# Performance work log

Measured on AMD Instinct MI355X. Metric: run time of the kernel, lower is better.

The kernel has to match this reference:

```python
import jax, jax.numpy as jnp
import numpy as np
import math

B, S = 4, 1024
V, D, L, H, F, MAXLEN = 32000, 1024, 6, 16, 4096, 2048
DH = D // H
NUM_BUCKETS, MAX_DIST = 32, 256
REL_SCALE = 64.0 ** 0.5
EPS = 1e-5


def setup_inputs() -> dict:
    key = jax.random.key(0)
    ks = iter(jax.random.split(key, 32))
    sd = 0.02
    inp = {
        'src': jax.random.randint(next(ks), (B, S), 0, V),
        'src_mask': jnp.ones((B, 1, 1, S), dtype=jnp.int32),
        'tok_emb': jax.random.normal(next(ks), (V, D), jnp.float32) * sd,
        'pos_emb': jax.random.normal(next(ks), (MAXLEN, D), jnp.float32) * sd,
        'Wq': jax.random.normal(next(ks), (L, D, D), jnp.float32) * sd,
        'bq': jnp.zeros((L, D), jnp.float32),
        'Wk': jax.random.normal(next(ks), (L, D, D), jnp.float32) * sd,
        'bk': jnp.zeros((L, D), jnp.float32),
        'Wv': jax.random.normal(next(ks), (L, D, D), jnp.float32) * sd,
        'bv': jnp.zeros((L, D), jnp.float32),
        'Wo': jax.random.normal(next(ks), (L, D, D), jnp.float32) * sd,
        'bo': jnp.zeros((L, D), jnp.float32),
        'rel_bias': jax.random.normal(next(ks), (L, NUM_BUCKETS, H), jnp.float32) * sd,
        'ln1_g': jnp.ones((L, D), jnp.float32),
        'ln1_b': jnp.zeros((L, D), jnp.float32),
        'W1': jax.random.normal(next(ks), (L, D, F), jnp.float32) * sd,
        'b1': jnp.zeros((L, F), jnp.float32),
        'W2': jax.random.normal(next(ks), (L, F, D), jnp.float32) * sd,
        'b2': jnp.zeros((L, D), jnp.float32),
        'ln2_g': jnp.ones((L, D), jnp.float32),
        'ln2_b': jnp.zeros((L, D), jnp.float32),
    }
    return inp


def _rel_pos_bucket(seq_len):
    # non-causal bucketing (T5-style), matching the torch source
    q = jnp.arange(seq_len)
    k = jnp.arange(seq_len)
    n = q[:, None] - k[None, :]          # == -(k - q)
    nb = NUM_BUCKETS // 2                # 16
    ret = (n < 0).astype(jnp.int32) * nb
    n = jnp.abs(n)
    max_exact = nb // 2                  # 8
    is_small = n < max_exact
    val_large = max_exact + (
        jnp.log(jnp.maximum(n, 1).astype(jnp.float32) / max_exact)
        / math.log(MAX_DIST / max_exact) * (nb - max_exact)
    ).astype(jnp.int32)
    val_large = jnp.minimum(val_large, nb - 1)
    return ret + jnp.where(is_small, n, val_large)  # [S,S] in [0,32)


def _layer_norm(x, g, b):
    mu = jnp.mean(x, axis=-1, keepdims=True)
    var = jnp.var(x, axis=-1, keepdims=True)
    return (x - mu) * jax.lax.rsqrt(var + EPS) * g + b


def reference(src, src_mask, tok_emb, pos_emb, Wq, bq, Wk, bk, Wv, bv, Wo, bo,
              rel_bias, ln1_g, ln1_b, W1, b1, W2, b2, ln2_g, ln2_b):
    seq_len = src.shape[1]
    bucket = _rel_pos_bucket(seq_len)                      # [S,S] int
    x = tok_emb[src] * jnp.sqrt(jnp.float32(D)) + pos_emb[jnp.arange(seq_len)][None]
    scale = jnp.sqrt(jnp.float32(DH))
    neg = jnp.float32(-1e10)

    def layer(x, p):
        (wq, bq_, wk, bk_, wv, bv_, wo, bo_, rb, g1, b1_, w1, bb1, w2, bb2, g2, b2_) = p
        Q = (x @ wq + bq_).reshape(B, seq_len, H, DH)
        K = (x @ wk + bk_).reshape(B, seq_len, H, DH)
        Vv = (x @ wv + bv_).reshape(B, seq_len, H, DH)
        energy = jnp.einsum('bqhd,bkhd->bhqk', Q, K) / scale
        energy = jnp.where(src_mask == 0, neg, energy)
        bias = rb[bucket]                                  # [S,S,H]
        energy = energy + jnp.transpose(bias, (2, 0, 1))[None] * REL_SCALE
        attn = jax.nn.softmax(energy, axis=-1)
        o = jnp.einsum('bhqk,bkhd->bqhd', attn, Vv).reshape(B, seq_len, D)
        o = o @ wo + bo_
        x = _layer_norm(x + o, g1, b1_)
        f = jax.nn.relu(x @ w1 + bb1) @ w2 + bb2
        x = _layer_norm(x + f, g2, b2_)
        return x, None

    params = (Wq, bq, Wk, bk, Wv, bv, Wo, bo, rel_bias,
              ln1_g, ln1_b, W1, b1, W2, b2, ln2_g, ln2_b)
    x, _ = jax.lax.scan(layer, x, params)
    return x
```

## Files before the change

### kernel.cpp

```cpp
#include <hip/hip_runtime.h>

#define B_ 4
#define S_ 1024
#define D_ 1024
#define F_ 4096
#define H_ 16
#define L_ 6
#define M_ (B_*S_)

#define LOG2E 1.44269504088896f

typedef unsigned short u16;
typedef __attribute__((ext_vector_type(4))) unsigned short u16x4;
typedef __attribute__((ext_vector_type(8))) short s16x8;
typedef __attribute__((ext_vector_type(8))) __bf16 bf16x8;
typedef __attribute__((ext_vector_type(4))) float f32x4;

typedef const __attribute__((address_space(1))) unsigned int gu32;
typedef __attribute__((address_space(3))) unsigned int su32;

__device__ __forceinline__ u16 f2bf(float f) {
  union { float f; unsigned u; } v; v.f = f;
  unsigned u = v.u;
  return (u16)((u + 0x7fffu + ((u >> 16) & 1u)) >> 16);
}
__device__ __forceinline__ float bf2f(u16 h) {
  union { unsigned u; float f; } v; v.u = (unsigned)h << 16; return v.f;
}

__device__ __forceinline__ f32x4 mfma16(s16x8 a, s16x8 b, f32x4 c) {
  return __builtin_amdgcn_mfma_f32_16x16x32_bf16(
      __builtin_bit_cast(bf16x8, a), __builtin_bit_cast(bf16x8, b), c, 0, 0, 0);
}

__device__ __forceinline__ void gload16(const void* g, void* s) {
  __builtin_amdgcn_global_load_lds((gu32*)g, (su32*)s, 16, 0, 0);
}

template<int OUTMODE>
__device__ __forceinline__ void gemm128_body(
    const u16* __restrict__ A, const u16* __restrict__ Bt,
    const float* __restrict__ b0, const float* __restrict__ b1,
    const float* __restrict__ b2, u16* __restrict__ Ch,
    u16* __restrict__ Vt, int N, int K, int kbeg, int kend)
{
  __shared__ __align__(16) u16 As[128 * 64];
  __shared__ __align__(16) u16 Bs[128 * 64];
  const int tid = threadIdx.x, lane = tid & 63, w = tid >> 6;
  const int bm = blockIdx.x * 128, bn = blockIdx.y * 128;
  const int wm = (w >> 1) * 64, wn = (w & 1) * 64;

  f32x4 acc[4][4];
#pragma unroll
  for (int i = 0; i < 4; i++)
#pragma unroll
    for (int j = 0; j < 4; j++) acc[i][j] = {0.f, 0.f, 0.f, 0.f};

  for (int k0 = kbeg; k0 < kend; k0 += 64) {
    __syncthreads();
#pragma unroll
    for (int i = 0; i < 4; i++) {
      const int flat = i * 4096 + w * 1024 + lane * 16;
      const int row = flat >> 7, ce = (flat & 127) >> 1;
      gload16(A + (size_t)(bm + row) * K + k0 + ce, As + i * 2048 + w * 512);
      gload16(Bt + (size_t)(bn + row) * K + k0 + ce, Bs + i * 2048 + w * 512);
    }
    __syncthreads();
#pragma unroll
    for (int kk = 0; kk < 2; kk++) {
      s16x8 af[4], bf[4];
#pragma unroll
      for (int mf = 0; mf < 4; mf++)
        af[mf] = *(const s16x8*)&As[(wm + mf * 16 + (lane & 15)) * 64 + kk * 32 + (lane >> 4) * 8];
#pragma unroll
      for (int nf = 0; nf < 4; nf++)
        bf[nf] = *(const s16x8*)&Bs[(wn + nf * 16 + (lane & 15)) * 64 + kk * 32 + (lane >> 4) * 8];
#pragma unroll
      for (int mf = 0; mf < 4; mf++)
#pragma unroll
        for (int nf = 0; nf < 4; nf++)
          acc[mf][nf] = mfma16(af[mf], bf[nf], acc[mf][nf]);
    }
  }

  if (OUTMODE == 3) {
    const int zz = bn >> 10;
    const int lcb = (bn & 1023) + wn;
    const float* bp = (zz == 0) ? b0 : (zz == 1) ? b1 : b2;
    if (zz == 2) {
      const int b = bm >> 10;
#pragma unroll
      for (int nf = 0; nf < 4; nf++) {
        const int dh2 = lcb + nf * 16 + (lane & 15);
        const int hq = dh2 >> 6, dh = dh2 & 63;
        const float bv = bp[dh2];
        u16* vrow = Vt + ((size_t)((b << 4) + hq) * 64 + dh) * S_;
#pragma unroll
        for (int mf = 0; mf < 4; mf++) {
          const int s0 = (bm & 1023) + wm + mf * 16 + ((lane >> 4) << 2);
          u16x4 hv;
#pragma unroll
          for (int j = 0; j < 4; j++) hv[j] = f2bf(acc[mf][nf][j] + bv);
          *(u16x4*)(vrow + s0) = hv;
        }
      }
    } else {
      const float sc = (zz == 0) ? (0.125f * LOG2E) : 1.0f;
      u16* Outz = Ch + (size_t)zz * M_ * D_;
#pragma unroll
      for (int nf = 0; nf < 4; nf++) {
        const int col = lcb + nf * 16 + (lane & 15);
        const float bv = bp[col];
#pragma unroll
        for (int mf = 0; mf < 4; mf++) {
#pragma unroll
          for (int j = 0; j < 4; j++) {
            const int row = bm + wm + mf * 16 + ((lane >> 4) << 2) + j;
            Outz[(size_t)row * D_ + col] = f2bf((acc[mf][nf][j] + bv) * sc);
          }
        }
      }
    }
  } else {
#pragma unroll
    for (int nf = 0; nf < 4; nf++) {
      const int col = bn + wn + nf * 16 + (lane & 15);
#pragma unroll
      for (int mf = 0; mf < 4; mf++) {
#pragma unroll
        for (int j = 0; j < 4; j++) {
          const int row = bm + wm + mf * 16 + ((lane >> 4) << 2) + j;
          Ch[(size_t)row * N + col] = f2bf(acc[mf][nf][j]);
        }
      }
    }
  }
}

__global__ __launch_bounds__(256, 3) void gemm_qkvf(
    const u16* __restrict__ A, const u16* __restrict__ WT,
    const float* __restrict__ bq, const float* __restrict__ bk,
    const float* __restrict__ bv, u16* __restrict__ Out, u16* __restrict__ Vt)
{
  gemm128_body<3>(A, WT, bq, bk, bv, Out, Vt, 3 * D_, D_, 0, D_);
}

__global__ __launch_bounds__(256, 3) void gemm_osplit2(
    const u16* __restrict__ A, const u16* __restrict__ WT,
    u16* __restrict__ P)
{
  const int z = blockIdx.z;
  gemm128_body<1>(A, WT, nullptr, nullptr, nullptr,
                  P + (size_t)z * M_ * D_, nullptr, D_, D_, z * 512, z * 512 + 512);
}

__device__ __forceinline__ s16x8 readfrag(const u16* half, int r, int kk, int hi4) {
  const int c = (kk * 64 + hi4 * 16) ^ ((r & 7) << 4);
  return *(const s16x8*)((const char*)half + r * 128 + c);
}

__device__ __forceinline__ void stage_half(
    const u16* __restrict__ src, int ldk, u16* lds_half, int w, int lane)
{
#pragma unroll
  for (int j = 0; j < 2; j++) {
    const int flat = j * 8192 + w * 1024 + lane * 16;
    const int row = flat >> 7;
    const int kb = (flat & 127) ^ ((row & 7) << 4);
    gload16(src + (size_t)row * ldk + (kb >> 1), lds_half + j * 4096 + w * 512);
  }
}

#define BAR     asm volatile("s_barrier" ::: "memory")
#define PH_PRE  asm volatile("s_barrier" ::: "memory"); __builtin_amdgcn_s_setprio(1)
#define PH_POST __builtin_amdgcn_s_setprio(0); __builtin_amdgcn_sched_barrier(0)
#define VM4     asm volatile("s_waitcnt vmcnt(4)" ::: "memory")
#define VM0     asm volatile("s_waitcnt vmcnt(0)" ::: "memory")

#define READ_B(bufhalf) do { \
  _Pragma("unroll") for (int nf = 0; nf < 4; nf++) \
  _Pragma("unroll") for (int kk = 0; kk < 2; kk++) \
    bfr[nf][kk] = readfrag(bufhalf, rb0 + nf * 16 + lo16, kk, hi4); } while (0)
#define READ_A(bufhalf, Q) do { \
  _Pragma("unroll") for (int m = 0; m < 2; m++) \
  _Pragma("unroll") for (int kk = 0; kk < 2; kk++) \
    af[m][kk] = readfrag(bufhalf, (2 * (Q) + m) * 16 + lo16, kk, hi4); } while (0)
#define DO_MFMA(Q) do { \
  _Pragma("unroll") for (int kk = 0; kk < 2; kk++) \
  _Pragma("unroll") for (int m = 0; m < 2; m++) \
  _Pragma("unroll") for (int nf = 0; nf < 4; nf++) \
    acc[2 * (Q) + m][nf] = mfma16(af[m][kk], bfr[nf][kk], acc[2 * (Q) + m][nf]); } while (0)

template<int OUTMODE>
__device__ __forceinline__ void gemm256_body(
    const u16* __restrict__ A, const u16* __restrict__ Bt,
    const float* __restrict__ bias, u16* __restrict__ Ch,
    int N, int K, int kbeg, int kslice)
{
  __shared__ __align__(16) u16 As[2][2][8192];
  __shared__ __align__(16) u16 Bs[2][2][8192];
  const int tid = threadIdx.x, lane = tid & 63, w = tid >> 6;
  const int wr = w >> 2, wc = w & 3;
  const int lo16 = lane & 15, hi4 = lane >> 4;
  const int bm = blockIdx.x * 256, bn = blockIdx.y * 256;
  const int rb0 = (wc & 1) * 64;

  const u16* Abase = A + (size_t)bm * K + kbeg;
  const u16* Bbase = Bt + (size_t)bn * K + kbeg;
  const size_t h1 = (size_t)128 * K;
  const int NT = kslice >> 6, NI = NT >> 1;

  f32x4 acc[8][4];
#pragma unroll
  for (int i = 0; i < 8; i++)
#pragma unroll
    for (int j = 0; j < 4; j++) acc[i][j] = {0.f, 0.f, 0.f, 0.f};

  stage_half(Abase,           K, As[0][0], w, lane);
  stage_half(Abase + h1,      K, As[0][1], w, lane);
  stage_half(Bbase,           K, Bs[0][0], w, lane);
  stage_half(Bbase + h1,      K, Bs[0][1], w, lane);
  stage_half(Abase + 64,      K, As[1][0], w, lane);
  stage_half(Abase + h1 + 64, K, As[1][1], w, lane);
  stage_half(Bbase + 64,      K, Bs[1][0], w, lane);
  stage_half(Bbase + h1 + 64, K, Bs[1][1], w, lane);
  asm volatile("s_waitcnt vmcnt(8)" ::: "memory");
  BAR;

  const u16* Ae = As[0][wr]; const u16* Ao = As[1][wr];
  const u16* Be = Bs[0][wc >> 1]; const u16* Bo = Bs[1][wc >> 1];
  s16x8 af[2][2], bfr[4][2];

  for (int it = 0; it < NI - 1; ++it) {
    READ_B(Be); READ_A(Ae, 0);
    if (it > 0) {
      stage_half(Abase +      (size_t)(2 * it + 1) * 64, K, As[1][0], w, lane);
      stage_half(Abase + h1 + (size_t)(2 * it + 1) * 64, K, As[1][1], w, lane);
    }
    PH_PRE; DO_MFMA(0); PH_POST; BAR;
    READ_A(Ae, 1);
    stage_half(Bbase +      (size_t)(2 * it + 2) * 64, K, Bs[0][0], w, lane);
    PH_PRE; DO_MFMA(1); PH_POST; BAR;
    READ_A(Ae, 2);
    stage_half(Bbase + h1 + (size_t)(2 * it + 2) * 64, K, Bs[0][1], w, lane);
    PH_PRE; DO_MFMA(2); PH_POST; BAR;
    READ_A(Ae, 3);
    PH_PRE; DO_MFMA(3); PH_POST; VM4; BAR;
    READ_B(Bo); READ_A(Ao, 0);
    stage_half(Abase +      (size_t)(2 * it + 2) * 64, K, As[0][0], w, lane);
    stage_half(Abase + h1 + (size_t)(2 * it + 2) * 64, K, As[0][1], w, lane);
    PH_PRE; DO_MFMA(0); PH_POST; BAR;
    READ_A(Ao, 1);
    stage_half(Bbase +      (size_t)(2 * it + 3) * 64, K, Bs[1][0], w, lane);
    PH_PRE; DO_MFMA(1); PH_POST; BAR;
    READ_A(Ao, 2);
    stage_half(Bbase + h1 + (size_t)(2 * it + 3) * 64, K, Bs[1][1], w, lane);
    PH_PRE; DO_MFMA(2); PH_POST; BAR;
    READ_A(Ao, 3);
    PH_PRE; DO_MFMA(3); PH_POST; VM4; BAR;
  }
  READ_B(Be); READ_A(Ae, 0);
  stage_half(Abase +      (size_t)(NT - 1) * 64, K, As[1][0], w, lane);
  stage_half(Abase + h1 + (size_t)(NT - 1) * 64, K, As[1][1], w, lane);
  PH_PRE; DO_MFMA(0); PH_POST; BAR;
  READ_A(Ae, 1);             PH_PRE; DO_MFMA(1); PH_POST; BAR;
  READ_A(Ae, 2);             PH_PRE; DO_MFMA(2); PH_POST; BAR;
  READ_A(Ae, 3);             PH_PRE; DO_MFMA(3); PH_POST; VM0; BAR;
  READ_B(Bo); READ_A(Ao, 0); PH_PRE; DO_MFMA(0); PH_POST; BAR;
  READ_A(Ao, 1);             PH_PRE; DO_MFMA(1); PH_POST; BAR;
  READ_A(Ao, 2);             PH_PRE; DO_MFMA(2); PH_POST; BAR;
  READ_A(Ao, 3);             PH_PRE; DO_MFMA(3); PH_POST;

  const int row0 = bm + wr * 128, col0 = bn + wc * 64;
#pragma unroll
  for (int nf = 0; nf < 4; nf++) {
    const int col = col0 + nf * 16 + lo16;
    const float bv = (OUTMODE == 2) ? bias[col] : 0.f;
#pragma unroll
    for (int mf = 0; mf < 8; mf++) {
#pragma unroll
      for (int j = 0; j < 4; j++) {
        const int row = row0 + mf * 16 + hi4 * 4 + j;
        float v = acc[mf][nf][j];
        if (OUTMODE == 2) v = fmaxf(v + bv, 0.f);
        Ch[(size_t)row * N + col] = f2bf(v);
      }
    }
  }
}

__global__ __launch_bounds__(512, 2) void gemm_ffn1(
    const u16* __restrict__ A, const u16* __restrict__ WT,
    const float* __restrict__ bias, u16* __restrict__ Out)
{
  gemm256_body<2>(A, WT, bias, Out, F_, D_, 0, D_);
}

__global__ __launch_bounds__(512, 2) void gemm_ffn2sp4(
    const u16* __restrict__ A, const u16* __restrict__ WT,
    u16* __restrict__ P)
{
  const int z = blockIdx.z;
  gemm256_body<4>(A, WT, nullptr, P + (size_t)z * M_ * D_,
                  D_, F_, z * 1024, 1024);
}

__global__ __launch_bounds__(256) void transpose_layer(
    const float* __restrict__ Wq, const float* __restrict__ Wk,
    const float* __restrict__ Wv, const float* __restrict__ Wo,
    const float* __restrict__ W1, const float* __restrict__ W2,
    u16* __restrict__ WT)
{
  __shared__ float tl[64][65];
  int bt = blockIdx.x;
  const float* src; u16* dst; int Rsrc, Csrc, cx, cy;
  if (bt < 1024) {
    const int m = bt >> 8; const int t = bt & 255;
    src = (m == 0) ? Wq : (m == 1) ? Wk : (m == 2) ? Wv : Wo;
    dst = WT + (size_t)m * 1024 * 1024;
    Rsrc = 1024; Csrc = 1024; cx = t & 15; cy = t >> 4;
  } else if (bt < 2048) {
    const int t = bt - 1024;
    src = W1; dst = WT + (size_t)4 * 1024 * 1024;
    Rsrc = 1024; Csrc = 4096; cx = t & 63; cy = t >> 6;
  } else {
    const int t = bt - 2048;
    src = W2; dst = WT + (size_t)8 * 1024 * 1024;
    Rsrc = 4096; Csrc = 1024; cx = t & 15; cy = t >> 4;
  }
  const int r0 = cy * 64, c0 = cx * 64;
  const int tid = threadIdx.x;
  const int rl = tid >> 2, q = tid & 3;
  const float* sp = src + (size_t)(r0 + rl) * Csrc + c0 + q * 16;
#pragma unroll
  for (int i = 0; i < 4; i++) {
    const float4 v = *(const float4*)(sp + i * 4);
    tl[rl][q * 16 + i * 4 + 0] = v.x;
    tl[rl][q * 16 + i * 4 + 1] = v.y;
    tl[rl][q * 16 + i * 4 + 2] = v.z;
    tl[rl][q * 16 + i * 4 + 3] = v.w;
  }
  __syncthreads();
#pragma unroll
  for (int it = 0; it < 2; it++) {
    const int idx = tid + it * 256;
    const int cl = idx >> 3, seg = idx & 7;
    const int rw0 = seg * 8;
    s16x8 v8;
#pragma unroll
    for (int u = 0; u < 8; u++) v8[u] = (short)f2bf(tl[rw0 + u][cl]);
    *(s16x8*)(dst + (size_t)(c0 + cl) * Rsrc + r0 + rw0) = v8;
  }
}

__global__ __launch_bounds__(256) void build_lut(
    const float* __restrict__ rb, float* __restrict__ lut_g)
{
  const int h = blockIdx.x, l = blockIdx.y;
  for (int idx = threadIdx.x; idx < 2048; idx += 256) {
    const int rel = idx - 1024;
    const int ret = rel < 0 ? 16 : 0;
    const int n = rel < 0 ? -rel : rel;
    int bu;
    if (n < 8) bu = ret + n;
    else {
      const float t = logf((float)n * 0.125f) * (8.0f / 3.4657359027997265f);
      int vl = 8 + (int)t;
      if (vl > 15) vl = 15;
      bu = ret + vl;
    }
    lut_g[(size_t)(l * H_ + h) * 2048 + idx] = rb[l * 512 + bu * 16 + h] * (8.0f * LOG2E);
  }
}

__global__ __launch_bounds__(256) void mask2neg(
    const int* __restrict__ mask, u16* __restrict__ mf)
{
  const int i = blockIdx.x * 256 + threadIdx.x;
  if (i < B_ * S_) mf[i] = mask[i] ? (u16)0 : f2bf(-1e10f * LOG2E);
}

__device__ __forceinline__ s16x8 lds_swz(const u16* base, int row, int cb) {
  const int addr = row * 128 + (cb ^ ((row & 7) << 4));
  return *(const s16x8*)((const char*)base + addr);
}

#define ATTN_STAGE(t, buf) do { \
  const int kt2 = (t) * 64; \
  const int flat2 = tid * 16; \
  const int row2 = flat2 >> 7; \
  const int ce2 = ((flat2 & 127) ^ ((row2 & 7) << 4)) >> 1; \
  gload16(Kb + (size_t)(bS + kt2 + row2) * D_ + hh + ce2, Ks[buf] + w * 512); \
  gload16(Vt + (size_t)(bh * 64 + row2) * S_ + kt2 + ce2, Vs[buf] + w * 512); \
} while (0)

#define ATTN_TILE(bc, kt) do { \
    f32x4 sacc[4]; \
    _Pragma("unroll") for (int i = 0; i < 4; i++) sacc[i] = {0.f, 0.f, 0.f, 0.f}; \
    __builtin_amdgcn_s_setprio(1); \
    _Pragma("unroll") for (int kk = 0; kk < 2; kk++) { \
      const int cb = kk * 64 + hi4 * 16; \
      _Pragma("unroll") for (int nf = 0; nf < 4; nf++) { \
        const s16x8 kb = lds_swz(Ks[bc], nf * 16 + lo16, cb); \
        sacc[nf] = mfma16(qf[kk], kb, sacc[nf]); \
      } \
    } \
    __builtin_amdgcn_s_setprio(0); \
    float kmf[4]; \
    _Pragma("unroll") for (int nf = 0; nf < 4; nf++) \
      kmf[nf] = bf2f(maskf[(kt) + nf * 16 + lo16]); \
    const int lidx0 = q0 + hi4 * 4 + 1024 - (kt) - lo16; \
    _Pragma("unroll") for (int j = 0; j < 4; j++) { \
      const int lrow = (hi4 << 2) + j; \
      _Pragma("unroll") for (int nf = 0; nf < 4; nf++) { \
        const float s = sacc[nf][j] + kmf[nf] + lut[lidx0 + j - nf * 16]; \
        Ps[w][lrow * 68 + nf * 16 + lo16] = f2bf(__builtin_amdgcn_exp2f(s)); \
      } \
    } \
    __builtin_amdgcn_s_setprio(1); \
    _Pragma("unroll") for (int kk = 0; kk < 2; kk++) { \
      const s16x8 pa = *(const s16x8*)&Ps[w][lo16 * 68 + kk * 32 + hi4 * 8]; \
      const int cb = kk * 64 + hi4 * 16; \
      _Pragma("unroll") for (int df = 0; df < 4; df++) { \
        const s16x8 vb = lds_swz(Vs[bc], df * 16 + lo16, cb); \
        oacc[df] = mfma16(pa, vb, oacc[df]); \
      } \
      oacc[4] = mfma16(pa, onesf, oacc[4]); \
    } \
    __builtin_amdgcn_s_setprio(0); \
} while (0)

__global__ __launch_bounds__(512, 2) void attn_kernel(
    const u16* __restrict__ Qb, const u16* __restrict__ Kb,
    const u16* __restrict__ Vt, const u16* __restrict__ mask16,
    const float* __restrict__ lut_g, u16* __restrict__ AO)
{
  __shared__ __align__(16) float lut[2048];
  __shared__ __align__(16) u16 maskf[1024];
  __shared__ __align__(16) u16 Ks[3][64 * 64];
  __shared__ __align__(16) u16 Vs[3][64 * 64];
  __shared__ __align__(16) u16 Ps[8][16 * 68];

  const int tid = threadIdx.x;
  const int lane = tid & 63;
  const int w = tid >> 6;
  const int bh = blockIdx.x;
  const int b = bh >> 4, h = bh & 15;
  const int q0 = blockIdx.y * 128 + w * 16;
  const int bS = b * S_, hh = h * 64;
  const int lo16 = lane & 15, hi4 = lane >> 4;

  const float* lsrc = lut_g + (size_t)h * 2048;
  gload16(lsrc + w * 256 + lane * 4, lut + w * 256);
  if (w < 2)
    gload16(mask16 + bS + w * 512 + lane * 8, maskf + w * 512);

  s16x8 qf[2];
#pragma unroll
  for (int kk = 0; kk < 2; kk++)
    qf[kk] = *(const s16x8*)(Qb + (size_t)(bS + q0 + lo16) * D_ + hh +
                             kk * 32 + hi4 * 8);

  s16x8 onesf;
#pragma unroll
  for (int u = 0; u < 8; u++) onesf[u] = (short)((lo16 == 0) ? 0x3F80 : 0);

  f32x4 oacc[5];
#pragma unroll
  for (int i = 0; i < 5; i++) oacc[i] = {0.f, 0.f, 0.f, 0.f};

  ATTN_STAGE(0, 0);
  ATTN_STAGE(1, 1);

  for (int t = 0; t < S_ / 64 - 1; ++t) {
    const int bc = t % 3;
    const int kt = t * 64;
    asm volatile("s_waitcnt vmcnt(2)" ::: "memory");
    __builtin_amdgcn_s_barrier();
    if (t + 2 < S_ / 64) ATTN_STAGE(t + 2, (t + 2) % 3);
    ATTN_TILE(bc, kt);
  }
  {
    const int t = S_ / 64 - 1;
    asm volatile("s_waitcnt vmcnt(0)" ::: "memory");
    __builtin_amdgcn_s_barrier();
    ATTN_TILE(t % 3, t * 64);
  }

  float inv[4];
#pragma unroll
  for (int j = 0; j < 4; j++) {
    const float l = __shfl(oacc[4][j], lane & 48);
    inv[j] = 1.0f / l;
  }
#pragma unroll
  for (int df = 0; df < 4; df++)
#pragma unroll
    for (int j = 0; j < 4; j++) {
      const int qrow = q0 + (hi4 << 2) + j;
      AO[(size_t)(bS + qrow) * D_ + hh + df * 16 + lo16] =
          f2bf(oacc[df][j] * inv[j]);
    }
}

template<int NP>
__global__ __launch_bounds__(256) void ln_fusedb(
    const u16* __restrict__ Xh, const u16* __restrict__ P,
    const float* __restrict__ bias, const float* __restrict__ g,
    const float* __restrict__ be, u16* __restrict__ Yh, float* __restrict__ Yf)
{
  const int row = blockIdx.x;
  const int tid = threadIdx.x;
  const size_t off = (size_t)row * D_;
  const size_t ps = (size_t)M_ * D_;
  const u16x4 xv = ((const u16x4*)(Xh + off))[tid];
  float v[4];
#pragma unroll
  for (int q = 0; q < 4; q++) v[q] = bf2f(xv[q]);
#pragma unroll
  for (int p = 0; p < NP; p++) {
    const u16x4 pv = ((const u16x4*)(P + p * ps + off))[tid];
#pragma unroll
    for (int q = 0; q < 4; q++) v[q] += bf2f(pv[q]);
  }
  const float4 bb = ((const float4*)bias)[tid];
  v[0] += bb.x; v[1] += bb.y; v[2] += bb.z; v[3] += bb.w;

  float sum = v[0] + v[1] + v[2] + v[3];
  float ss = v[0] * v[0] + v[1] * v[1] + v[2] * v[2] + v[3] * v[3];
#pragma unroll
  for (int o = 1; o < 64; o <<= 1) {
    sum += __shfl_xor(sum, o);
    ss += __shfl_xor(ss, o);
  }
  __shared__ float s1[4], s2[4];
  if ((tid & 63) == 0) { s1[tid >> 6] = sum; s2[tid >> 6] = ss; }
  __syncthreads();
  sum = s1[0] + s1[1] + s1[2] + s1[3];
  ss = s2[0] + s2[1] + s2[2] + s2[3];
  const float mu = sum * (1.f / D_);
  const float var = ss * (1.f / D_) - mu * mu;
  const float rstd = rsqrtf(var + 1e-5f);
  const float4 gv = ((const float4*)g)[tid];
  const float4 bv = ((const float4*)be)[tid];
  float y[4];
  y[0] = (v[0] - mu) * rstd * gv.x + bv.x;
  y[1] = (v[1] - mu) * rstd * gv.y + bv.y;
  y[2] = (v[2] - mu) * rstd * gv.z + bv.z;
  y[3] = (v[3] - mu) * rstd * gv.w + bv.w;
  u16x4 hv;
  hv.x = f2bf(y[0]); hv.y = f2bf(y[1]); hv.z = f2bf(y[2]); hv.w = f2bf(y[3]);
  ((u16x4*)(Yh + off))[tid] = hv;
  if (Yf != nullptr) {
    float4 yf; yf.x = y[0]; yf.y = y[1]; yf.z = y[2]; yf.w = y[3];
    ((float4*)(Yf + off))[tid] = yf;
  }
}

__global__ __launch_bounds__(256) void embed_kernel(
    const int* __restrict__ src, const float* __restrict__ tok,
    const float* __restrict__ pos, u16* __restrict__ Xh)
{
  const int row = blockIdx.x;
  const int s = row & (S_ - 1);
  const int t = src[row];
  const int tid = threadIdx.x;
  const float4 tv = ((const float4*)(tok + (size_t)t * D_))[tid];
  const float4 pv = ((const float4*)(pos + (size_t)s * D_))[tid];
  u16x4 hv;
  hv.x = f2bf(tv.x * 32.f + pv.x);
  hv.y = f2bf(tv.y * 32.f + pv.y);
  hv.z = f2bf(tv.z * 32.f + pv.z);
  hv.w = f2bf(tv.w * 32.f + pv.w);
  ((u16x4*)(Xh + (size_t)row * D_))[tid] = hv;
}

extern "C" void kernel_launch(void* const* d_in, const int* in_sizes, int n_in,
                              void* d_out, int out_size, void* d_ws, size_t ws_size,
                              hipStream_t stream)
{
  const int* src = (const int*)d_in[0];
  const int* mask = (const int*)d_in[1];
  const float* tok_emb = (const float*)d_in[2];
  const float* pos_emb = (const float*)d_in[3];
  const float* Wq = (const float*)d_in[4];
  const float* bq = (const float*)d_in[5];
  const float* Wk = (const float*)d_in[6];
  const float* bk = (const float*)d_in[7];
  const float* Wv = (const float*)d_in[8];
  const float* bv = (const float*)d_in[9];
  const float* Wo = (const float*)d_in[10];
  const float* bo = (const float*)d_in[11];
  const float* rb = (const float*)d_in[12];
  const float* g1 = (const float*)d_in[13];
  const float* b1n = (const float*)d_in[14];
  const float* W1 = (const float*)d_in[15];
  const float* b1f = (const float*)d_in[16];
  const float* W2 = (const float*)d_in[17];
  const float* b2f = (const float*)d_in[18];
  const float* g2 = (const float*)d_in[19];
  const float* b2n = (const float*)d_in[20];
  float* out = (float*)d_out;

  char* ws = (char*)d_ws;
  const size_t MB = 1ull << 20;
  u16* xb16  = (u16*)(ws + 0);
  u16* Qb16  = (u16*)(ws + 8 * MB);
  u16* Kb16  = (u16*)(ws + 16 * MB);
  u16* Vt16  = (u16*)(ws + 24 * MB);
  u16* AO16  = (u16*)(ws + 32 * MB);
  u16* Pp16  = (u16*)(ws + 40 * MB);
  u16* WT    = (u16*)(ws + 72 * MB);
  u16* Hb16  = (u16*)(ws + 8 * MB);
  float* lut_g  = (float*)(ws + 96 * MB);
  u16*   mask16 = (u16*)(ws + 96 * MB + 786432);

  u16* WTqkv = WT;
  u16* WTo   = WT + (size_t)3 * 1024 * 1024;
  u16* WT1   = WT + (size_t)4 * 1024 * 1024;
  u16* WT2   = WT + (size_t)8 * 1024 * 1024;

  embed_kernel<<<M_, 256, 0, stream>>>(src, tok_emb, pos_emb, xb16);
  build_lut<<<dim3(H_, L_), 256, 0, stream>>>(rb, lut_g);
  mask2neg<<<(B_ * S_ + 255) / 256, 256, 0, stream>>>(mask, mask16);

  for (int l = 0; l < L_; l++) {
    const size_t oDD = (size_t)l * D_ * D_;
    const size_t oDF = (size_t)l * D_ * F_;

    transpose_layer<<<3072, 256, 0, stream>>>(
        Wq + oDD, Wk + oDD, Wv + oDD, Wo + oDD, W1 + oDF, W2 + oDF, WT);

    gemm_qkvf<<<dim3(M_ / 128, 3 * D_ / 128), 256, 0, stream>>>(
        xb16, WTqkv, bq + l * D_, bk + l * D_, bv + l * D_, Qb16, Vt16);

    attn_kernel<<<dim3(B_ * H_, S_ / 128), 512, 0, stream>>>(
        Qb16, Kb16, Vt16, mask16, lut_g + (size_t)l * H_ * 2048, AO16);

    gemm_osplit2<<<dim3(M_ / 128, D_ / 128, 2), 256, 0, stream>>>(
        AO16, WTo, Pp16);

    ln_fusedb<2><<<M_, 256, 0, stream>>>(
        xb16, Pp16, bo + l * D_, g1 + l * D_, b1n + l * D_, xb16, nullptr);

    gemm_ffn1<<<dim3(M_ / 256, F_ / 256), 512, 0, stream>>>(
        xb16, WT1, b1f + l * F_, Hb16);

    gemm_ffn2sp4<<<dim3(M_ / 256, D_ / 256, 4), 512, 0, stream>>>(
        Hb16, WT2, Pp16);

    ln_fusedb<4><<<M_, 256, 0, stream>>>(
        xb16, Pp16, b2f + l * D_, g2 + l * D_, b2n + l * D_, xb16,
        (l == L_ - 1) ? out : nullptr);
  }
}
```

Measured before the change: 1.233 ms.

## Replace 128x128 QKV/out-proj GEMM with pipelined 256x128 double-buffered tile

The QKV and output-projection GEMMs move from a simple 128x128 tile, which synchronises twice per K step with no prefetch, to a 256x128 tile run by 512 threads. The new body double-buffers LDS with swizzled staging and overlaps the next tile's global-to-LDS loads with MFMA phases, using barriers and setprio. This is meant to hide load latency and raise reuse of operands per byte loaded. In exchange it needs more LDS per block and allows fewer resident blocks, and the grid has half as many blocks, which may hurt wave balance across CUs.

Measured after the change: 1.261 ms. 2.3% more time.

```diff
diff --git a/kernel.cpp b/kernel.cpp
--- a/kernel.cpp
+++ b/kernel.cpp
@@ -37,18 +37,65 @@
   __builtin_amdgcn_global_load_lds((gu32*)g, (su32*)s, 16, 0, 0);
 }
 
+__device__ __forceinline__ s16x8 readfrag(const u16* half, int r, int kk, int hi4) {
+  const int c = (kk * 64 + hi4 * 16) ^ ((r & 7) << 4);
+  return *(const s16x8*)((const char*)half + r * 128 + c);
+}
+
+__device__ __forceinline__ void stage_half(
+    const u16* __restrict__ src, int ldk, u16* lds_half, int w, int lane)
+{
+#pragma unroll
+  for (int j = 0; j < 2; j++) {
+    const int flat = j * 8192 + w * 1024 + lane * 16;
+    const int row = flat >> 7;
+    const int kb = (flat & 127) ^ ((row & 7) << 4);
+    gload16(src + (size_t)row * ldk + (kb >> 1), lds_half + j * 4096 + w * 512);
+  }
+}
+
+#define BAR     asm volatile("s_barrier" ::: "memory")
+#define PH_PRE  asm volatile("s_barrier" ::: "memory"); __builtin_amdgcn_s_setprio(1)
+#define PH_POST __builtin_amdgcn_s_setprio(0); __builtin_amdgcn_sched_barrier(0)
+#define VM0     asm volatile("s_waitcnt vmcnt(0)" ::: "memory")
+#define VM2     asm volatile("s_waitcnt vmcnt(2)" ::: "memory")
+#define VM4     asm volatile("s_waitcnt vmcnt(4)" ::: "memory")
+
+#define READ_BX(buf) do { \
+  _Pragma("unroll") for (int nf = 0; nf < 4; nf++) \
+  _Pragma("unroll") for (int kk = 0; kk < 2; kk++) \
+    bfr[nf][kk] = readfrag(buf, rb0 + nf * 16 + lo16, kk, hi4); } while (0)
+#define READ_AX(buf, Q0) do { \
+  _Pragma("unroll") for (int m = 0; m < 2; m++) \
+  _Pragma("unroll") for (int kk = 0; kk < 2; kk++) \
+    af[m][kk] = readfrag(buf, ar0 + ((Q0) + m) * 16 + lo16, kk, hi4); } while (0)
+#define DO_MFMAX(Q0) do { \
+  _Pragma("unroll") for (int kk = 0; kk < 2; kk++) \
+  _Pragma("unroll") for (int m = 0; m < 2; m++) \
+  _Pragma("unroll") for (int nf = 0; nf < 4; nf++) \
+    acc[(Q0) + m][nf] = mfma16(af[m][kk], bfr[nf][kk], acc[(Q0) + m][nf]); } while (0)
+
 template<int OUTMODE>
-__device__ __forceinline__ void gemm128_body(
+__device__ __forceinline__ void gemm256x128_body(
     const u16* __restrict__ A, const u16* __restrict__ Bt,
     const float* __restrict__ b0, const float* __restrict__ b1,
     const float* __restrict__ b2, u16* __restrict__ Ch,
-    u16* __restrict__ Vt, int N, int K, int kbeg, int kend)
-{
-  __shared__ __align__(16) u16 As[128 * 64];
-  __shared__ __align__(16) u16 Bs[128 * 64];
+    u16* __restrict__ Vt, int N, int K, int kbeg, int kslice)
+{
+  __shared__ __align__(16) u16 As[2][2][8192];
+  __shared__ __align__(16) u16 Bs[2][8192];
   const int tid = threadIdx.x, lane = tid & 63, w = tid >> 6;
-  const int bm = blockIdx.x * 128, bn = blockIdx.y * 128;
-  const int wm = (w >> 1) * 64, wn = (w & 1) * 64;
+  const int wr = w >> 1, wc = w & 1;
+  const int lo16 = lane & 15, hi4 = lane >> 4;
+  const int bm = blockIdx.x * 256, bn = blockIdx.y * 128;
+  const int ah = wr >> 1;
+  const int ar0 = (wr & 1) * 64;
+  const int rb0 = wc * 64;
+
+  const u16* Abase = A + (size_t)bm * K + kbeg;
+  const u16* Bbase = Bt + (size_t)bn * K + kbeg;
+  const size_t h1 = (size_t)128 * K;
+  const int NT = kslice >> 6, NI = NT >> 1;
 
   f32x4 acc[4][4];
 #pragma unroll
@@ -56,48 +103,62 @@
 #pragma unroll
     for (int j = 0; j < 4; j++) acc[i][j] = {0.f, 0.f, 0.f, 0.f};
 
-  for (int k0 = kbeg; k0 < kend; k0 += 64) {
-    __syncthreads();
-#pragma unroll
-    for (int i = 0; i < 4; i++) {
-      const int flat = i * 4096 + w * 1024 + lane * 16;
-      const int row = flat >> 7, ce = (flat & 127) >> 1;
-      gload16(A + (size_t)(bm + row) * K + k0 + ce, As + i * 2048 + w * 512);
-      gload16(Bt + (size_t)(bn + row) * K + k0 + ce, Bs + i * 2048 + w * 512);
+  stage_half(Abase,           K, As[0][0], w, lane);
+  stage_half(Abase + h1,      K, As[0][1], w, lane);
+  stage_half(Bbase,           K, Bs[0],    w, lane);
+  stage_half(Abase + 64,      K, As[1][0], w, lane);
+  stage_half(Abase + h1 + 64, K, As[1][1], w, lane);
+  stage_half(Bbase + 64,      K, Bs[1],    w, lane);
+  asm volatile("s_waitcnt vmcnt(6)" ::: "memory");
+  BAR;
+
+  s16x8 af[2][2], bfr[4][2];
+
+  for (int it = 0; it < NI - 1; ++it) {
+    READ_BX(Bs[0]); READ_AX(As[0][ah], 0);
+    if (it > 0) {
+      stage_half(Abase +      (size_t)(2 * it + 1) * 64, K, As[1][0], w, lane);
+      stage_half(Abase + h1 + (size_t)(2 * it + 1) * 64, K, As[1][1], w, lane);
     }
-    __syncthreads();
-#pragma unroll
-    for (int kk = 0; kk < 2; kk++) {
-      s16x8 af[4], bf[4];
-#pragma unroll
-      for (int mf = 0; mf < 4; mf++)
-        af[mf] = *(const s16x8*)&As[(wm + mf * 16 + (lane & 15)) * 64 + kk * 32 + (lane >> 4) * 8];
-#pragma unroll
-      for (int nf = 0; nf < 4; nf++)
-        bf[nf] = *(const s16x8*)&Bs[(wn + nf * 16 + (lane & 15)) * 64 + kk * 32 + (lane >> 4) * 8];
-#pragma unroll
-      for (int mf = 0; mf < 4; mf++)
-#pragma unroll
-        for (int nf = 0; nf < 4; nf++)
-          acc[mf][nf] = mfma16(af[mf], bf[nf], acc[mf][nf]);
-    }
-  }
-
+    PH_PRE; DO_MFMAX(0); PH_POST; BAR;
+    READ_AX(As[0][ah], 2);
+    stage_half(Bbase + (size_t)(2 * it + 2) * 64, K, Bs[0], w, lane);
+    PH_PRE; DO_MFMAX(2); PH_POST; VM2; BAR;
+    READ_BX(Bs[1]); READ_AX(As[1][ah], 0);
+    stage_half(Abase +      (size_t)(2 * it + 2) * 64, K, As[0][0], w, lane);
+    stage_half(Abase + h1 + (size_t)(2 * it + 2) * 64, K, As[0][1], w, lane);
+    PH_PRE; DO_MFMAX(0); PH_POST; BAR;
+    READ_AX(As[1][ah], 2);
+    stage_half(Bbase + (size_t)(2 * it + 3) * 64, K, Bs[1], w, lane);
+    PH_PRE; DO_MFMAX(2); PH_POST; VM2; BAR;
+  }
+  READ_BX(Bs[0]); READ_AX(As[0][ah], 0);
+  stage_half(Abase +      (size_t)(NT - 1) * 64, K, As[1][0], w, lane);
+  stage_half(Abase + h1 + (size_t)(NT - 1) * 64, K, As[1][1], w, lane);
+  PH_PRE; DO_MFMAX(0); PH_POST; BAR;
+  READ_AX(As[0][ah], 2);
+  PH_PRE; DO_MFMAX(2); PH_POST; VM0; BAR;
+  READ_BX(Bs[1]); READ_AX(As[1][ah], 0);
+  PH_PRE; DO_MFMAX(0); PH_POST; BAR;
+  READ_AX(As[1][ah], 2);
+  PH_PRE; DO_MFMAX(2); PH_POST;
+
+  const int row0 = bm + wr * 64;
   if (OUTMODE == 3) {
     const int zz = bn >> 10;
-    const int lcb = (bn & 1023) + wn;
+    const int lcb = (bn & 1023) + wc * 64;
     const float* bp = (zz == 0) ? b0 : (zz == 1) ? b1 : b2;
     if (zz == 2) {
       const int b = bm >> 10;
 #pragma unroll
       for (int nf = 0; nf < 4; nf++) {
-        const int dh2 = lcb + nf * 16 + (lane & 15);
+        const int dh2 = lcb + nf * 16 + lo16;
         const int hq = dh2 >> 6, dh = dh2 & 63;
         const float bv = bp[dh2];
         u16* vrow = Vt + ((size_t)((b << 4) + hq) * 64 + dh) * S_;
 #pragma unroll
         for (int mf = 0; mf < 4; mf++) {
-          const int s0 = (bm & 1023) + wm + mf * 16 + ((lane >> 4) << 2);
+          const int s0 = (row0 & 1023) + mf * 16 + (hi4 << 2);
           u16x4 hv;
 #pragma unroll
           for (int j = 0; j < 4; j++) hv[j] = f2bf(acc[mf][nf][j] + bv);
@@ -109,13 +170,13 @@
       u16* Outz = Ch + (size_t)zz * M_ * D_;
 #pragma unroll
       for (int nf = 0; nf < 4; nf++) {
-        const int col = lcb + nf * 16 + (lane & 15);
+        const int col = lcb + nf * 16 + lo16;
         const float bv = bp[col];
 #pragma unroll
         for (int mf = 0; mf < 4; mf++) {
 #pragma unroll
           for (int j = 0; j < 4; j++) {
-            const int row = bm + wm + mf * 16 + ((lane >> 4) << 2) + j;
+            const int row = row0 + mf * 16 + (hi4 << 2) + j;
             Outz[(size_t)row * D_ + col] = f2bf((acc[mf][nf][j] + bv) * sc);
           }
         }
@@ -124,12 +185,12 @@
   } else {
 #pragma unroll
     for (int nf = 0; nf < 4; nf++) {
-      const int col = bn + wn + nf * 16 + (lane & 15);
+      const int col = bn + wc * 64 + nf * 16 + lo16;
 #pragma unroll
       for (int mf = 0; mf < 4; mf++) {
 #pragma unroll
         for (int j = 0; j < 4; j++) {
-          const int row = bm + wm + mf * 16 + ((lane >> 4) << 2) + j;
+          const int row = row0 + mf * 16 + (hi4 << 2) + j;
           Ch[(size_t)row * N + col] = f2bf(acc[mf][nf][j]);
         }
       }
@@ -137,45 +198,22 @@
   }
 }
 
-__global__ __launch_bounds__(256, 3) void gemm_qkvf(
+__global__ __launch_bounds__(512, 2) void gemm_qkvf(
     const u16* __restrict__ A, const u16* __restrict__ WT,
     const float* __restrict__ bq, const float* __restrict__ bk,
     const float* __restrict__ bv, u16* __restrict__ Out, u16* __restrict__ Vt)
 {
-  gemm128_body<3>(A, WT, bq, bk, bv, Out, Vt, 3 * D_, D_, 0, D_);
-}
-
-__global__ __launch_bounds__(256, 3) void gemm_osplit2(
+  gemm256x128_body<3>(A, WT, bq, bk, bv, Out, Vt, 3 * D_, D_, 0, D_);
+}
+
+__global__ __launch_bounds__(512, 2) void gemm_osplit2(
     const u16* __restrict__ A, const u16* __restrict__ WT,
     u16* __restrict__ P)
 {
   const int z = blockIdx.z;
-  gemm128_body<1>(A, WT, nullptr, nullptr, nullptr,
-                  P + (size_t)z * M_ * D_, nullptr, D_, D_, z * 512, z * 512 + 512);
-}
-
-__device__ __forceinline__ s16x8 readfrag(const u16* half, int r, int kk, int hi4) {
-  const int c = (kk * 64 + hi4 * 16) ^ ((r & 7) << 4);
-  return *(const s16x8*)((const char*)half + r * 128 + c);
-}
-
-__device__ __forceinline__ void stage_half(
-    const u16* __restrict__ src, int ldk, u16* lds_half, int w, int lane)
-{
-#pragma unroll
-  for (int j = 0; j < 2; j++) {
-    const int flat = j * 8192 + w * 1024 + lane * 16;
-    const int row = flat >> 7;
-    const int kb = (flat & 127) ^ ((row & 7) << 4);
-    gload16(src + (size_t)row * ldk + (kb >> 1), lds_half + j * 4096 + w * 512);
-  }
-}
-
-#define BAR     asm volatile("s_barrier" ::: "memory")
-#define PH_PRE  asm volatile("s_barrier" ::: "memory"); __builtin_amdgcn_s_setprio(1)
-#define PH_POST __builtin_amdgcn_s_setprio(0); __builtin_amdgcn_sched_barrier(0)
-#define VM4     asm volatile("s_waitcnt vmcnt(4)" ::: "memory")
-#define VM0     asm volatile("s_waitcnt vmcnt(0)" ::: "memory")
+  gemm256x128_body<1>(A, WT, nullptr, nullptr, nullptr,
+                      P + (size_t)z * M_ * D_, nullptr, D_, D_, z * 512, 512);
+}
 
 #define READ_B(bufhalf) do { \
   _Pragma("unroll") for (int nf = 0; nf < 4; nf++) \
@@ -631,13 +669,13 @@
     transpose_layer<<<3072, 256, 0, stream>>>(
         Wq + oDD, Wk + oDD, Wv + oDD, Wo + oDD, W1 + oDF, W2 + oDF, WT);
 
-    gemm_qkvf<<<dim3(M_ / 128, 3 * D_ / 128), 256, 0, stream>>>(
+    gemm_qkvf<<<dim3(M_ / 256, 3 * D_ / 128), 512, 0, stream>>>(
         xb16, WTqkv, bq + l * D_, bk + l * D_, bv + l * D_, Qb16, Vt16);
 
     attn_kernel<<<dim3(B_ * H_, S_ / 128), 512, 0, stream>>>(
         Qb16, Kb16, Vt16, mask16, lut_g + (size_t)l * H_ * 2048, AO16);
 
-    gemm_osplit2<<<dim3(M_ / 128, D_ / 128, 2), 256, 0, stream>>>(
+    gemm_osplit2<<<dim3(M_ / 256, D_ / 128, 2), 512, 0, stream>>>(
         AO16, WTo, Pp16);
 
     ln_fusedb<2><<<M_, 256, 0, stream>>>(
```
